# Kernel tuning notes

Measured on AMD Instinct MI355X. Metric: run time of the kernel, lower is better.

Reference implementation:

```python
import jax, jax.numpy as jnp
import numpy as np

B, H, E, K = 8192, 1024, 8, 2


def setup_inputs() -> dict:
    key = jax.random.key(0)
    k1, k2, k3 = jax.random.split(key, 3)
    x = jax.random.normal(k1, (B, H), dtype=jnp.float32)
    gate_w = jax.random.normal(k2, (H, E), dtype=jnp.float32) / np.sqrt(H)
    expert_w = jax.random.normal(k3, (E, H, H), dtype=jnp.float32) / np.sqrt(H)
    return {"x": x, "gate_w": gate_w, "expert_w": expert_w}


def reference(x, gate_w, expert_w):
    # Gate: logits over experts, top-k routing, softmax over the k selected logits
    logits = x @ gate_w                               # [B, E]
    top_w, top_idx = jax.lax.top_k(logits, K)         # [B, K]
    top_w = jax.nn.softmax(top_w, axis=-1)            # softmax over the K selected
    # Combine weights scattered back to [B, E]; zero for unselected experts
    combine = jnp.zeros((x.shape[0], expert_w.shape[0]), dtype=x.dtype)
    combine = combine.at[jnp.arange(x.shape[0])[:, None], top_idx].add(top_w)
    # Expert GEMMs (dense dispatch reference: every expert on every token,
    # masked/weighted by combine; mathematically identical to gather/scatter)
    expert_out = jnp.einsum('bh,eho->beo', x, expert_w)   # [B, E, H]
    out = jnp.einsum('be,beo->bo', combine, expert_out)   # [B, H]
    return out
```

## Files before the change

### kernel.cpp

```cpp
#include <hip/hip_runtime.h>
#include <hip/hip_bf16.h>
#include <stdint.h>

#define B_TOK 8192
#define H_DIM 1024
#define E_NUM 8
#define NSLOT (2 * B_TOK)

typedef __attribute__((ext_vector_type(8))) short short8;
typedef __attribute__((ext_vector_type(4))) float floatx4;

__device__ __forceinline__ unsigned short f32_to_bf16_rne(float f) {
  union { float f; uint32_t u; } v; v.f = f;
  uint32_t u = v.u;
  uint32_t r = u + 0x7FFFu + ((u >> 16) & 1u);
  return (unsigned short)(r >> 16);
}
__device__ __forceinline__ float bf16_to_f32(unsigned short s) {
  union { uint32_t u; float f; } v; v.u = ((uint32_t)s) << 16;
  return v.f;
}

__global__ __launch_bounds__(256) void transpose_w_kernel(const float* __restrict__ w,
                                                          unsigned short* __restrict__ wt) {
  __shared__ float tile[32][33];
  int e = blockIdx.z;
  int n0 = blockIdx.x * 32, k0 = blockIdx.y * 32;
  int tx = threadIdx.x, ty = threadIdx.y;
  const float* wb = w + (size_t)e * H_DIM * H_DIM;
  unsigned short* wtb = wt + (size_t)e * H_DIM * H_DIM;
#pragma unroll
  for (int j = 0; j < 4; j++) {
    int r = ty + j * 8;
    tile[r][tx] = wb[(size_t)(k0 + r) * H_DIM + n0 + tx];
  }
  __syncthreads();
#pragma unroll
  for (int j = 0; j < 4; j++) {
    int r = ty + j * 8;
    wtb[(size_t)(n0 + r) * H_DIM + k0 + tx] = f32_to_bf16_rne(tile[tx][r]);
  }
}

__global__ __launch_bounds__(256) void route_kernel(const float* __restrict__ x,
                                                    const float* __restrict__ gw,
                                                    unsigned short* __restrict__ xb,
                                                    int2* __restrict__ re,
                                                    float2* __restrict__ rw) {
  __shared__ float gws[E_NUM][1028];
  int tid = threadIdx.x;
#pragma unroll
  for (int it = 0; it < 8; ++it) {
    int i4 = it * 256 + tid;
    float4 v = ((const float4*)gw)[i4];
    int h = i4 >> 1, e0 = (i4 & 1) * 4;
    gws[e0 + 0][h] = v.x;
    gws[e0 + 1][h] = v.y;
    gws[e0 + 2][h] = v.z;
    gws[e0 + 3][h] = v.w;
  }
  __syncthreads();
  int wid = tid >> 6, lane = tid & 63;
  for (int t = 0; t < 8; ++t) {
    int b = blockIdx.x * 32 + wid * 8 + t;
    const float4* xr = (const float4*)(x + (size_t)b * H_DIM);
    ushort4* xbr = (ushort4*)(xb + (size_t)b * H_DIM);
    float acc[E_NUM];
#pragma unroll
    for (int e = 0; e < E_NUM; e++) acc[e] = 0.f;
#pragma unroll
    for (int it = 0; it < 4; ++it) {
      int c4 = it * 64 + lane;
      float4 v = xr[c4];
      ushort4 o;
      o.x = f32_to_bf16_rne(v.x); o.y = f32_to_bf16_rne(v.y);
      o.z = f32_to_bf16_rne(v.z); o.w = f32_to_bf16_rne(v.w);
      xbr[c4] = o;
      int h = c4 * 4;
#pragma unroll
      for (int e = 0; e < E_NUM; e++) {
        float4 g = *(const float4*)&gws[e][h];
        acc[e] += v.x * g.x + v.y * g.y + v.z * g.z + v.w * g.w;
      }
    }
#pragma unroll
    for (int e = 0; e < E_NUM; e++) {
#pragma unroll
      for (int off = 32; off; off >>= 1) acc[e] += __shfl_xor(acc[e], off, 64);
    }
    if (lane == 0) {
      int e0 = 0; float v0 = acc[0];
#pragma unroll
      for (int e = 1; e < E_NUM; e++) if (acc[e] > v0) { v0 = acc[e]; e0 = e; }
      int e1 = -1; float v1 = -1e30f;
#pragma unroll
      for (int e = 0; e < E_NUM; e++) if (e != e0 && acc[e] > v1) { v1 = acc[e]; e1 = e; }
      float s = expf(v1 - v0);
      float w0 = 1.0f / (1.0f + s);
      re[b] = make_int2(e0, e1);
      rw[b] = make_float2(w0, s * w0);
    }
  }
}

__global__ __launch_bounds__(1024) void compact_kernel(const int2* __restrict__ re,
                                                       int* __restrict__ slot_tok,
                                                       int* __restrict__ yslot,
                                                       int* __restrict__ ebase,
                                                       int* __restrict__ ecnt) {
  __shared__ int wcnt[16];
  int e = blockIdx.x;
  int tid = threadIdx.x, wid = tid >> 6, lane = tid & 63;
  int c = 0;
#pragma unroll
  for (int it = 0; it < 8; ++it) {
    int2 ee = re[it * 1024 + tid];
    c += (ee.x < e) + (ee.y < e);
  }
#pragma unroll
  for (int off = 32; off; off >>= 1) c += __shfl_xor(c, off, 64);
  if (lane == 0) wcnt[wid] = c;
  __syncthreads();
  int base = 0;
#pragma unroll
  for (int i = 0; i < 16; ++i) base += wcnt[i];
  __syncthreads();
  int run = 0;
  for (int it = 0; it < 8; ++it) {
    int t = it * 1024 + tid;
    int2 ee = re[t];
    bool f0 = (ee.x == e), f1 = (ee.y == e);
    bool f = f0 || f1;
    unsigned long long m = __ballot(f);
    int pre = __popcll(m & ((1ull << lane) - 1ull));
    if (lane == 0) wcnt[wid] = __popcll(m);
    __syncthreads();
    int wbase = 0, total = 0;
#pragma unroll
    for (int i = 0; i < 16; ++i) { int v = wcnt[i]; if (i < wid) wbase += v; total += v; }
    if (f) {
      int s = base + run + wbase + pre;
      slot_tok[s] = t;
      yslot[2 * t + (f0 ? 0 : 1)] = s;
    }
    run += total;
    __syncthreads();
  }
  if (tid == 0) { ebase[e] = base; ecnt[e] = run; }
}

__device__ __forceinline__ void async_ld16(const void* g, void* l) {
  __builtin_amdgcn_global_load_lds((const __attribute__((address_space(1))) void*)g,
                                   (__attribute__((address_space(3))) void*)l, 16, 0, 0);
}

__global__ __launch_bounds__(256, 2) void moe_gemm_kernel(
    const unsigned short* __restrict__ xb,
    const unsigned short* __restrict__ wt,
    const int* __restrict__ ebase,
    const int* __restrict__ ecnt,
    const int* __restrict__ slot_tok,
    unsigned short* __restrict__ y) {
  int e = blockIdx.z;
  int c = ecnt[e];
  int m0 = blockIdx.y * 128;
  if (m0 >= c) return;
  int base = ebase[e];
  int n0 = blockIdx.x * 128;

  __shared__ __align__(16) unsigned short As[128 * 32];
  __shared__ __align__(16) unsigned short Bs[128 * 32];

  int tid = threadIdx.x, wid = tid >> 6, lane = tid & 63;
  int rs = wid * 16 + (lane >> 2);
  int kc = (lane & 3) * 8;
  const int* st = slot_tok + base;
  int ra1 = min(m0 + rs, c - 1);
  int ra2 = min(m0 + 64 + rs, c - 1);
  const unsigned short* gA1 = xb + (size_t)st[ra1] * H_DIM + kc;
  const unsigned short* gA2 = xb + (size_t)st[ra2] * H_DIM + kc;
  const unsigned short* gB1 = wt + ((size_t)e * H_DIM + n0 + rs) * H_DIM + kc;
  const unsigned short* gB2 = wt + ((size_t)e * H_DIM + n0 + 64 + rs) * H_DIM + kc;
  unsigned short* lA1 = As + wid * 512;
  unsigned short* lA2 = As + 2048 + wid * 512;
  unsigned short* lB1 = Bs + wid * 512;
  unsigned short* lB2 = Bs + 2048 + wid * 512;

  floatx4 acc[4][4];
#pragma unroll
  for (int a = 0; a < 4; ++a)
#pragma unroll
    for (int b = 0; b < 4; ++b)
#pragma unroll
      for (int q = 0; q < 4; ++q) acc[a][b][q] = 0.0f;

  int wm = (wid >> 1) * 64, wn = (wid & 1) * 64;
  int mr = lane & 15, kg = lane >> 4;

  for (int ks = 0; ks < H_DIM / 32; ++ks) {
    __syncthreads();
    async_ld16(gA1, lA1);
    async_ld16(gA2, lA2);
    async_ld16(gB1, lB1);
    async_ld16(gB2, lB2);
    gA1 += 32; gA2 += 32; gB1 += 32; gB2 += 32;
    __syncthreads();
    short8 af[4], bfr[4];
#pragma unroll
    for (int t = 0; t < 4; ++t) {
      af[t] = *(const short8*)(const void*)(As + (wm + t * 16 + mr) * 32 + kg * 8);
      bfr[t] = *(const short8*)(const void*)(Bs + (wn + t * 16 + mr) * 32 + kg * 8);
    }
#pragma unroll
    for (int tm = 0; tm < 4; ++tm)
#pragma unroll
      for (int tn = 0; tn < 4; ++tn)
        acc[tm][tn] = __builtin_amdgcn_mfma_f32_16x16x32_bf16(af[tm], bfr[tn], acc[tm][tn], 0, 0, 0);
  }

#pragma unroll
  for (int tm = 0; tm < 4; ++tm) {
#pragma unroll
    for (int q = 0; q < 4; ++q) {
      int r = m0 + wm + tm * 16 + kg * 4 + q;
      if (r < c) {
        unsigned short* yrow = y + (size_t)(base + r) * H_DIM + n0 + wn + mr;
#pragma unroll
        for (int tn = 0; tn < 4; ++tn) yrow[tn * 16] = f32_to_bf16_rne(acc[tm][tn][q]);
      }
    }
  }
}

__global__ __launch_bounds__(256) void combine_kernel(const unsigned short* __restrict__ y,
                                                      const int* __restrict__ yslot,
                                                      const float2* __restrict__ rw,
                                                      float* __restrict__ out) {
  int t = blockIdx.x;
  int s0 = yslot[2 * t], s1 = yslot[2 * t + 1];
  float2 w = rw[t];
  const ushort4* y0 = (const ushort4*)(y + (size_t)s0 * H_DIM);
  const ushort4* y1 = (const ushort4*)(y + (size_t)s1 * H_DIM);
  float4* o = (float4*)(out + (size_t)t * H_DIM);
  int i = threadIdx.x;
  ushort4 a = y0[i], b = y1[i];
  float4 r;
  r.x = w.x * bf16_to_f32(a.x) + w.y * bf16_to_f32(b.x);
  r.y = w.x * bf16_to_f32(a.y) + w.y * bf16_to_f32(b.y);
  r.z = w.x * bf16_to_f32(a.z) + w.y * bf16_to_f32(b.z);
  r.w = w.x * bf16_to_f32(a.w) + w.y * bf16_to_f32(b.w);
  o[i] = r;
}

extern "C" void kernel_launch(void* const* d_in, const int* in_sizes, int n_in,
                              void* d_out, int out_size, void* d_ws, size_t ws_size,
                              hipStream_t stream) {
  const float* x  = (const float*)d_in[0];
  const float* gw = (const float*)d_in[1];
  const float* ew = (const float*)d_in[2];
  float* out = (float*)d_out;

  char* ws = (char*)d_ws;
  unsigned short* xb = (unsigned short*)ws;
  unsigned short* wt = (unsigned short*)(ws + (size_t)16 * 1024 * 1024);
  unsigned short* y  = (unsigned short*)(ws + (size_t)32 * 1024 * 1024);
  char* p = ws + (size_t)64 * 1024 * 1024;
  int2*   re       = (int2*)p;
  float2* rw       = (float2*)(p + (64 << 10));
  int*    slot_tok = (int*)(p + (128 << 10));
  int*    yslot    = (int*)(p + (192 << 10));
  int*    ebase    = (int*)(p + (256 << 10));
  int*    ecnt     = (int*)(p + (256 << 10) + 64);

  transpose_w_kernel<<<dim3(32, 32, E_NUM), dim3(32, 8), 0, stream>>>(ew, wt);
  route_kernel<<<256, 256, 0, stream>>>(x, gw, xb, re, rw);
  compact_kernel<<<E_NUM, 1024, 0, stream>>>(re, slot_tok, yslot, ebase, ecnt);
  moe_gemm_kernel<<<dim3(H_DIM / 128, B_TOK / 128, E_NUM), 256, 0, stream>>>(
      xb, wt, ebase, ecnt, slot_tok, y);
  combine_kernel<<<B_TOK, 256, 0, stream>>>(y, yslot, rw, out);
}
```

Measured before the change: 194.2 us.

## Vectorize weight transpose, swizzle GEMM LDS, remap GEMM grid, streamline compaction

```diff
diff --git a/kernel.cpp b/kernel.cpp
--- a/kernel.cpp
+++ b/kernel.cpp
@@ -23,22 +23,29 @@
 
 __global__ __launch_bounds__(256) void transpose_w_kernel(const float* __restrict__ w,
                                                           unsigned short* __restrict__ wt) {
-  __shared__ float tile[32][33];
+  __shared__ float tile[64][68];
   int e = blockIdx.z;
-  int n0 = blockIdx.x * 32, k0 = blockIdx.y * 32;
-  int tx = threadIdx.x, ty = threadIdx.y;
-  const float* wb = w + (size_t)e * H_DIM * H_DIM;
-  unsigned short* wtb = wt + (size_t)e * H_DIM * H_DIM;
-#pragma unroll
-  for (int j = 0; j < 4; j++) {
-    int r = ty + j * 8;
-    tile[r][tx] = wb[(size_t)(k0 + r) * H_DIM + n0 + tx];
+  int k0 = blockIdx.y * 64, n0 = blockIdx.x * 64;
+  const float* wb = w + ((size_t)e * H_DIM + k0) * H_DIM + n0;
+  unsigned short* wtb = wt + ((size_t)e * H_DIM + n0) * H_DIM + k0;
+  int t = threadIdx.x;
+  int rr = t >> 4, c4 = t & 15;
+#pragma unroll
+  for (int j = 0; j < 4; ++j) {
+    int r = rr + j * 16;
+    float4 v = *(const float4*)(wb + (size_t)r * H_DIM + c4 * 4);
+    *(float4*)&tile[r][c4 * 4] = v;
   }
   __syncthreads();
 #pragma unroll
-  for (int j = 0; j < 4; j++) {
-    int r = ty + j * 8;
-    wtb[(size_t)(n0 + r) * H_DIM + k0 + tx] = f32_to_bf16_rne(tile[tx][r]);
+  for (int j = 0; j < 4; ++j) {
+    int nr = rr + j * 16;
+    ushort4 o;
+    o.x = f32_to_bf16_rne(tile[c4 * 4 + 0][nr]);
+    o.y = f32_to_bf16_rne(tile[c4 * 4 + 1][nr]);
+    o.z = f32_to_bf16_rne(tile[c4 * 4 + 2][nr]);
+    o.w = f32_to_bf16_rne(tile[c4 * 4 + 3][nr]);
+    *(ushort4*)(wtb + (size_t)nr * H_DIM + c4 * 4) = o;
   }
 }
 
@@ -61,8 +68,8 @@
   }
   __syncthreads();
   int wid = tid >> 6, lane = tid & 63;
-  for (int t = 0; t < 8; ++t) {
-    int b = blockIdx.x * 32 + wid * 8 + t;
+  for (int t = 0; t < 4; ++t) {
+    int b = blockIdx.x * 16 + wid * 4 + t;
     const float4* xr = (const float4*)(x + (size_t)b * H_DIM);
     ushort4* xbr = (ushort4*)(xb + (size_t)b * H_DIM);
     float acc[E_NUM];
@@ -108,43 +115,43 @@
                                                        int* __restrict__ yslot,
                                                        int* __restrict__ ebase,
                                                        int* __restrict__ ecnt) {
-  __shared__ int wcnt[16];
+  __shared__ int wcnt[8][16];
+  __shared__ int bless[16];
   int e = blockIdx.x;
   int tid = threadIdx.x, wid = tid >> 6, lane = tid & 63;
-  int c = 0;
+  int cless = 0;
+  int flag[8];
+  unsigned long long mm[8];
 #pragma unroll
   for (int it = 0; it < 8; ++it) {
     int2 ee = re[it * 1024 + tid];
-    c += (ee.x < e) + (ee.y < e);
-  }
-#pragma unroll
-  for (int off = 32; off; off >>= 1) c += __shfl_xor(c, off, 64);
-  if (lane == 0) wcnt[wid] = c;
+    cless += (ee.x < e) + (ee.y < e);
+    bool f0 = (ee.x == e), f1 = (ee.y == e);
+    flag[it] = f0 ? 1 : (f1 ? 2 : 0);
+    mm[it] = __ballot(f0 || f1);
+    if (lane == 0) wcnt[it][wid] = __popcll(mm[it]);
+  }
+#pragma unroll
+  for (int off = 32; off; off >>= 1) cless += __shfl_xor(cless, off, 64);
+  if (lane == 0) bless[wid] = cless;
   __syncthreads();
   int base = 0;
 #pragma unroll
-  for (int i = 0; i < 16; ++i) base += wcnt[i];
-  __syncthreads();
+  for (int i = 0; i < 16; ++i) base += bless[i];
   int run = 0;
+#pragma unroll
   for (int it = 0; it < 8; ++it) {
-    int t = it * 1024 + tid;
-    int2 ee = re[t];
-    bool f0 = (ee.x == e), f1 = (ee.y == e);
-    bool f = f0 || f1;
-    unsigned long long m = __ballot(f);
-    int pre = __popcll(m & ((1ull << lane) - 1ull));
-    if (lane == 0) wcnt[wid] = __popcll(m);
-    __syncthreads();
     int wbase = 0, total = 0;
 #pragma unroll
-    for (int i = 0; i < 16; ++i) { int v = wcnt[i]; if (i < wid) wbase += v; total += v; }
-    if (f) {
+    for (int i = 0; i < 16; ++i) { int v = wcnt[it][i]; if (i < wid) wbase += v; total += v; }
+    if (flag[it]) {
+      int pre = __popcll(mm[it] & ((1ull << lane) - 1ull));
       int s = base + run + wbase + pre;
+      int t = it * 1024 + tid;
       slot_tok[s] = t;
-      yslot[2 * t + (f0 ? 0 : 1)] = s;
+      yslot[2 * t + (flag[it] == 1 ? 0 : 1)] = s;
     }
     run += total;
-    __syncthreads();
   }
   if (tid == 0) { ebase[e] = base; ecnt[e] = run; }
 }
@@ -154,7 +161,7 @@
                                    (__attribute__((address_space(3))) void*)l, 16, 0, 0);
 }
 
-__global__ __launch_bounds__(256, 2) void moe_gemm_kernel(
+__global__ __launch_bounds__(256, 4) void moe_gemm_kernel(
     const unsigned short* __restrict__ xb,
     const unsigned short* __restrict__ wt,
     const int* __restrict__ ebase,
@@ -163,17 +170,20 @@
     unsigned short* __restrict__ y) {
   int e = blockIdx.z;
   int c = ecnt[e];
-  int m0 = blockIdx.y * 128;
+  int m_idx = ((blockIdx.y >> 3) << 3) + blockIdx.x;
+  int n_idx = blockIdx.y & 7;
+  int m0 = m_idx * 128;
   if (m0 >= c) return;
   int base = ebase[e];
-  int n0 = blockIdx.x * 128;
+  int n0 = n_idx * 128;
 
   __shared__ __align__(16) unsigned short As[128 * 32];
   __shared__ __align__(16) unsigned short Bs[128 * 32];
 
   int tid = threadIdx.x, wid = tid >> 6, lane = tid & 63;
   int rs = wid * 16 + (lane >> 2);
-  int kc = (lane & 3) * 8;
+  int swz = (rs >> 1) & 3;
+  int kc = ((lane & 3) ^ swz) * 8;
   const int* st = slot_tok + base;
   int ra1 = min(m0 + rs, c - 1);
   int ra2 = min(m0 + 64 + rs, c - 1);
@@ -208,8 +218,10 @@
     short8 af[4], bfr[4];
 #pragma unroll
     for (int t = 0; t < 4; ++t) {
-      af[t] = *(const short8*)(const void*)(As + (wm + t * 16 + mr) * 32 + kg * 8);
-      bfr[t] = *(const short8*)(const void*)(Bs + (wn + t * 16 + mr) * 32 + kg * 8);
+      int rowa = wm + t * 16 + mr;
+      int rowb = wn + t * 16 + mr;
+      af[t]  = *(const short8*)(const void*)(As + rowa * 32 + ((kg ^ ((rowa >> 1) & 3)) * 8));
+      bfr[t] = *(const short8*)(const void*)(Bs + rowb * 32 + ((kg ^ ((rowb >> 1) & 3)) * 8));
     }
 #pragma unroll
     for (int tm = 0; tm < 4; ++tm)
@@ -272,10 +284,10 @@
   int*    ebase    = (int*)(p + (256 << 10));
   int*    ecnt     = (int*)(p + (256 << 10) + 64);
 
-  transpose_w_kernel<<<dim3(32, 32, E_NUM), dim3(32, 8), 0, stream>>>(ew, wt);
-  route_kernel<<<256, 256, 0, stream>>>(x, gw, xb, re, rw);
+  transpose_w_kernel<<<dim3(16, 16, E_NUM), 256, 0, stream>>>(ew, wt);
+  route_kernel<<<512, 256, 0, stream>>>(x, gw, xb, re, rw);
   compact_kernel<<<E_NUM, 1024, 0, stream>>>(re, slot_tok, yslot, ebase, ecnt);
-  moe_gemm_kernel<<<dim3(H_DIM / 128, B_TOK / 128, E_NUM), 256, 0, stream>>>(
+  moe_gemm_kernel<<<dim3(8, 64, E_NUM), 256, 0, stream>>>(
       xb, wt, ebase, ecnt, slot_tok, y);
   combine_kernel<<<B_TOK, 256, 0, stream>>>(y, yslot, rw, out);
 }
```

Result: faster. 182.9 us (-5.8%).
